# Kernel tuning notes

Hardware: AMD Instinct MI355X
Metric: run time of the kernel (lower is better)

Reference implementation:

```python
import jax, jax.numpy as jnp
import numpy as np

B, T, D, H = 4, 2048, 1024, 16
HD = D // H


def setup_inputs() -> dict:
    key = jax.random.key(0)
    ks = jax.random.split(key, 10)
    s = 1.0 / np.sqrt(D)
    # xavier_uniform bound for wbias [T,T]: sqrt(6/(T+T))
    wb_bound = float(np.sqrt(6.0 / (T + T)))
    return {
        "x": jax.random.normal(ks[0], (B, T, D), dtype=jnp.float32),
        "Wq": jax.random.normal(ks[1], (D, D), dtype=jnp.float32) * s,
        "bq": jnp.zeros((D,), dtype=jnp.float32),
        "Wk": jax.random.normal(ks[2], (D, D), dtype=jnp.float32) * s,
        "bk": jnp.zeros((D,), dtype=jnp.float32),
        "Wv": jax.random.normal(ks[3], (D, D), dtype=jnp.float32) * s,
        "bv": jnp.zeros((D,), dtype=jnp.float32),
        "Wo": jax.random.normal(ks[4], (D, D), dtype=jnp.float32) * s,
        "bo": jnp.zeros((D,), dtype=jnp.float32),
        "wbias": jax.random.uniform(ks[5], (T, T), dtype=jnp.float32,
                                    minval=-wb_bound, maxval=wb_bound),
    }


def reference(x, Wq, bq, Wk, bk, Wv, bv, Wo, bo, wbias):
    Bc, Tc, Dc = x.shape
    # projections, split heads: [B, H, T, HD]
    def proj(W, b):
        y = x @ W + b
        return y.reshape(Bc, Tc, H, HD).transpose(0, 2, 1, 3)

    Q = proj(Wq, bq)
    K = proj(Wk, bk)
    V = proj(Wv, bv)

    Q_sig = jax.nn.sigmoid(Q)
    eK = jnp.exp(K)                      # [B,H,T,HD]
    ew = jnp.exp(wbias[:Tc, :Tc])        # [T,T]

    num = jnp.einsum('ts,bhsd->bhtd', ew, eK * V)
    den = jnp.einsum('ts,bhsd->bhtd', ew, eK)
    out = Q_sig * (num / den)            # [B,H,T,HD]

    out = out.transpose(0, 2, 1, 3).reshape(Bc, Tc, Dc)
    return out @ Wo + bo
```

## Files before the change

kernel.cpp:

```cpp
#include <hip/hip_runtime.h>
#include <hip/hip_bf16.h>


#define AS1(p) ((const __attribute__((address_space(1))) void*)(p))
#define AS3(p) ((__attribute__((address_space(3))) void*)(p))

typedef _Float16 half8 __attribute__((ext_vector_type(8)));
typedef _Float16 half4v __attribute__((ext_vector_type(4)));
typedef float floatx16 __attribute__((ext_vector_type(16)));

__global__ void prep_cast_exp(const float* __restrict__ x, const float* __restrict__ wb,
                              _Float16* __restrict__ x_h, _Float16* __restrict__ ew_h) {
  int i = blockIdx.x * 256 + threadIdx.x;
  if (i < 2097152) {
    float4 v = ((const float4*)x)[i];
    half4v h;
    h[0] = (_Float16)v.x; h[1] = (_Float16)v.y; h[2] = (_Float16)v.z; h[3] = (_Float16)v.w;
    ((half4v*)x_h)[i] = h;
  } else {
    int j = i - 2097152;
    float4 v = ((const float4*)wb)[j];
    half4v h;
    h[0] = (_Float16)__expf(v.x); h[1] = (_Float16)__expf(v.y);
    h[2] = (_Float16)__expf(v.z); h[3] = (_Float16)__expf(v.w);
    ((half4v*)ew_h)[j] = h;
  }
}

__global__ void transpose_cast_w(const float* __restrict__ w0, const float* __restrict__ w1,
                                 const float* __restrict__ w2, const float* __restrict__ w3,
                                 _Float16* __restrict__ dqkv, _Float16* __restrict__ dwo) {
  const int z = blockIdx.z;
  const float* src = z == 0 ? w0 : z == 1 ? w1 : z == 2 ? w2 : w3;
  __shared__ float tile[32][33];
  const int r0 = blockIdx.x * 32, c0 = blockIdx.y * 32;
  const int tr = threadIdx.x >> 5, tc = threadIdx.x & 31;
#pragma unroll
  for (int p = 0; p < 4; ++p) {
    int rr = tr + p * 8;
    tile[rr][tc] = src[(size_t)(r0 + rr) * 1024 + c0 + tc];
  }
  __syncthreads();
#pragma unroll
  for (int p = 0; p < 4; ++p) {
    int c = c0 + tr + p * 8;
    size_t jr;
    _Float16* dst;
    if (z == 0) { jr = c; dst = dqkv; }
    else if (z == 3) { jr = c; dst = dwo; }
    else { jr = 1024 + ((size_t)(c >> 5) << 6) + ((z == 2) ? 32 : 0) + (c & 31); dst = dqkv; }
    dst[jr * 1024 + r0 + tc] = (_Float16)tile[tc][tr + p * 8];
  }
}

template <int MODE>
__global__ __launch_bounds__(256) void gemm_bt(
    const _Float16* __restrict__ A, const _Float16* __restrict__ Bt, void* __restrict__ Cv,
    int M, int N, int K, long batchB, long batchCbytes,
    const float* __restrict__ bias0, const float* __restrict__ bias1,
    const float* __restrict__ bias2, const _Float16* __restrict__ Qsig, long batchQ,
    _Float16* __restrict__ Zt) {
  __shared__ __align__(16) _Float16 sA[8192];
  __shared__ __align__(16) _Float16 sB[8192];
  const int tid = threadIdx.x;
  const int wave = tid >> 6, lane = tid & 63;
  const int l32 = lane & 31, khalf = lane >> 5;
  const int m0 = blockIdx.x * 128, n0 = blockIdx.y * 128;
  Bt += (long)blockIdx.z * batchB;
  char* Cb = (char*)Cv + (long)blockIdx.z * batchCbytes;

  const int rs = tid >> 3;
  const int ug = (tid & 7) ^ (rs & 7);
  const _Float16* gA = A + (long)(m0 + rs) * K + ug * 8;
  const _Float16* gB = Bt + (long)(n0 + rs) * K + ug * 8;
  _Float16* sAd = sA + wave * 512;
  _Float16* sBd = sB + wave * 512;

  const int wm = (wave >> 1) * 64, wn = (wave & 1) * 64;

  floatx16 acc[2][2] = {};

  for (int k0 = 0; k0 < K; k0 += 64) {
#pragma unroll
    for (int c = 0; c < 4; ++c)
      __builtin_amdgcn_global_load_lds(AS1(gA + (long)c * 32 * K + k0), AS3(sAd + c * 2048), 16,
                                       0, 0);
#pragma unroll
    for (int c = 0; c < 4; ++c)
      __builtin_amdgcn_global_load_lds(AS1(gB + (long)c * 32 * K + k0), AS3(sBd + c * 2048), 16,
                                       0, 0);
    __syncthreads();
#pragma unroll
    for (int ks = 0; ks < 4; ++ks) {
      half8 af[2], bf[2];
#pragma unroll
      for (int i = 0; i < 2; ++i) {
        int ra = wm + i * 32 + l32;
        af[i] = *(const half8*)(sA + ra * 64 + (((ks * 2 + khalf) ^ (ra & 7)) * 8));
        int rb = wn + i * 32 + l32;
        bf[i] = *(const half8*)(sB + rb * 64 + (((ks * 2 + khalf) ^ (rb & 7)) * 8));
      }
#pragma unroll
      for (int mt = 0; mt < 2; ++mt)
#pragma unroll
        for (int nt = 0; nt < 2; ++nt)
          acc[mt][nt] =
              __builtin_amdgcn_mfma_f32_32x32x16_f16(af[mt], bf[nt], acc[mt][nt], 0, 0, 0);
    }
    __syncthreads();
  }

  if (MODE == 0) {
    if (n0 < 1024) {
      _Float16* Qs = (_Float16*)Cb;
#pragma unroll
      for (int mt = 0; mt < 2; ++mt)
#pragma unroll
        for (int nt = 0; nt < 2; ++nt) {
          const int col = n0 + wn + nt * 32 + l32;
          const float bb = bias0[col];
#pragma unroll
          for (int reg = 0; reg < 16; ++reg) {
            const int row = m0 + wm + mt * 32 + 4 * khalf + 8 * (reg >> 2) + (reg & 3);
            float v = acc[mt][nt][reg] + bb;
            Qs[(long)row * 1024 + col] = (_Float16)(1.0f / (1.0f + __expf(-v)));
          }
        }
    } else {
      const int g = (n0 - 1024 + wn) >> 6;
      const int ch = g * 32 + l32;
      const float bkc = bias1[ch], bvc = bias2[ch];
#pragma unroll
      for (int mt = 0; mt < 2; ++mt) {
#pragma unroll
        for (int q = 0; q < 4; ++q) {
          half4v numv, denv;
#pragma unroll
          for (int r = 0; r < 4; ++r) {
            float ek = __expf(acc[mt][0][q * 4 + r] + bkc);
            float vv = acc[mt][1][q * 4 + r] + bvc;
            denv[r] = (_Float16)ek;
            numv[r] = (_Float16)(ek * vv);
          }
          const int row = m0 + wm + mt * 32 + 4 * khalf + 8 * q;
          const int b = row >> 11, s = row & 2047;
          const size_t jb = ((size_t)b * 2048 + (size_t)g * 64 + l32) * 2048 + s;
          *(half4v*)(Zt + jb) = numv;
          *(half4v*)(Zt + jb + 32 * 2048) = denv;
        }
      }
    }
    return;
  }

  if (MODE == 3) {
    const _Float16* Q = Qsig + (long)blockIdx.z * batchQ;
    const int ch = ((n0 + wn) >> 6) * 32 + l32;
#pragma unroll
    for (int mt = 0; mt < 2; ++mt)
#pragma unroll
      for (int reg = 0; reg < 16; ++reg) {
        const int row = m0 + wm + mt * 32 + 4 * khalf + 8 * (reg >> 2) + (reg & 3);
        float num = acc[mt][0][reg], den = acc[mt][1][reg];
        float qs = (float)Q[(long)row * 1024 + ch];
        ((_Float16*)Cb)[(long)row * 1024 + ch] = (_Float16)(qs * num / den);
      }
    return;
  }

#pragma unroll
  for (int mt = 0; mt < 2; ++mt)
#pragma unroll
    for (int nt = 0; nt < 2; ++nt) {
      const int col = n0 + wn + nt * 32 + l32;
      const float bb = bias0[col];
#pragma unroll
      for (int reg = 0; reg < 16; ++reg) {
        const int row = m0 + wm + mt * 32 + 4 * khalf + 8 * (reg >> 2) + (reg & 3);
        ((float*)Cb)[(long)row * N + col] = acc[mt][nt][reg] + bb;
      }
    }
}

extern "C" void kernel_launch(void* const* d_in, const int* in_sizes, int n_in, void* d_out,
                              int out_size, void* d_ws, size_t ws_size, hipStream_t stream) {
  const float* x = (const float*)d_in[0];
  const float* Wq = (const float*)d_in[1];
  const float* bq = (const float*)d_in[2];
  const float* Wk = (const float*)d_in[3];
  const float* bk = (const float*)d_in[4];
  const float* Wv = (const float*)d_in[5];
  const float* bv = (const float*)d_in[6];
  const float* Wo = (const float*)d_in[7];
  const float* bo = (const float*)d_in[8];
  const float* wb = (const float*)d_in[9];

  char* ws = (char*)d_ws;
  _Float16* x_h = (_Float16*)(ws + 0);
  _Float16* WqkvT = (_Float16*)(ws + 16777216);
  _Float16* WoT = (_Float16*)(ws + 23068672);
  _Float16* ew_h = (_Float16*)(ws + 25165824);
  _Float16* Qsig = (_Float16*)(ws + 33554432);
  _Float16* Zt = (_Float16*)(ws + 50331648);
  _Float16* OutHead = (_Float16*)(ws + 83886080);

  prep_cast_exp<<<12288, 256, 0, stream>>>(x, wb, x_h, ew_h);
  transpose_cast_w<<<dim3(32, 32, 4), 256, 0, stream>>>(Wq, Wk, Wv, Wo, WqkvT, WoT);

  gemm_bt<0><<<dim3(64, 24, 1), 256, 0, stream>>>(x_h, WqkvT, Qsig, 8192, 3072, 1024, 0, 0, bq,
                                                  bk, bv, nullptr, 0, Zt);

  gemm_bt<3><<<dim3(16, 16, 4), 256, 0, stream>>>(ew_h, Zt, OutHead, 2048, 2048, 2048,
                                                  (long)2048 * 2048, (long)2048 * 1024 * 2,
                                                  nullptr, nullptr, nullptr, Qsig,
                                                  (long)2048 * 1024, nullptr);

  gemm_bt<2><<<dim3(64, 8, 1), 256, 0, stream>>>(OutHead, WoT, d_out, 8192, 1024, 1024, 0, 0, bo,
                                                 nullptr, nullptr, nullptr, 0, nullptr);
}
```

Measured before the change: 302.0 us.

## Pre-tile GEMM operands into MFMA fragment order for contiguous tile loads

Every fp16 GEMM operand (x, exp(wbias), transposed weights, the num/den buffer and the per-head output) is now written in a blocked 128x64 tile layout whose element order matches the MFMA fragment order. The GEMM kernel can then fetch each K-tile with fully contiguous global-to-LDS loads and read fragments with plain lane-linear LDS reads, with no XOR swizzle or strided row addressing. The cost is scattered, narrower stores in the producer kernels and epilogues (the MODE 3 epilogue writes single halves to tiled addresses), and possible LDS bank conflicts.

Result: no change. 301.7 us (-0.1%).

```diff
diff --git a/kernel.cpp b/kernel.cpp
--- a/kernel.cpp
+++ b/kernel.cpp
@@ -9,21 +9,43 @@
 typedef _Float16 half4v __attribute__((ext_vector_type(4)));
 typedef float floatx16 __attribute__((ext_vector_type(16)));
 
-__global__ void prep_cast_exp(const float* __restrict__ x, const float* __restrict__ wb,
-                              _Float16* __restrict__ x_h, _Float16* __restrict__ ew_h) {
-  int i = blockIdx.x * 256 + threadIdx.x;
-  if (i < 2097152) {
-    float4 v = ((const float4*)x)[i];
-    half4v h;
-    h[0] = (_Float16)v.x; h[1] = (_Float16)v.y; h[2] = (_Float16)v.z; h[3] = (_Float16)v.w;
-    ((half4v*)x_h)[i] = h;
+__device__ __forceinline__ long frag_off(int r, int k) {
+  return (long)(((((r >> 5) * 4 + (k >> 4)) * 2 + ((k >> 3) & 1)) * 32 + (r & 31)) * 8 + (k & 7));
+}
+
+__global__ void prep_tiles(const float* __restrict__ x, const float* __restrict__ wb,
+                           _Float16* __restrict__ x_h, _Float16* __restrict__ ew_h) {
+  const int bid = blockIdx.x;
+  const int tid = threadIdx.x;
+  const bool isx = bid < 1024;
+  const float* src;
+  _Float16* dst;
+  int tm, tk, ld, trel;
+  if (isx) {
+    trel = bid; tm = bid >> 4; tk = bid & 15; src = x; dst = x_h; ld = 1024;
   } else {
-    int j = i - 2097152;
-    float4 v = ((const float4*)wb)[j];
-    half4v h;
-    h[0] = (_Float16)__expf(v.x); h[1] = (_Float16)__expf(v.y);
-    h[2] = (_Float16)__expf(v.z); h[3] = (_Float16)__expf(v.w);
-    ((half4v*)ew_h)[j] = h;
+    trel = bid - 1024; tm = trel >> 5; tk = trel & 31; src = wb; dst = ew_h; ld = 2048;
+  }
+  const long tbase = (long)trel * 8192;
+#pragma unroll
+  for (int p = 0; p < 4; ++p) {
+    const int s = p * 256 + tid;
+    const int r = ((s >> 8) << 5) + (s & 31);
+    const int k = ((s >> 6) & 3) * 16 + ((s >> 5) & 1) * 8;
+    const float* sp = src + (long)(tm * 128 + r) * ld + tk * 64 + k;
+    const float4 v0 = *(const float4*)sp;
+    const float4 v1 = *(const float4*)(sp + 4);
+    half8 h;
+    if (isx) {
+      h[0] = (_Float16)v0.x; h[1] = (_Float16)v0.y; h[2] = (_Float16)v0.z; h[3] = (_Float16)v0.w;
+      h[4] = (_Float16)v1.x; h[5] = (_Float16)v1.y; h[6] = (_Float16)v1.z; h[7] = (_Float16)v1.w;
+    } else {
+      h[0] = (_Float16)__expf(v0.x); h[1] = (_Float16)__expf(v0.y);
+      h[2] = (_Float16)__expf(v0.z); h[3] = (_Float16)__expf(v0.w);
+      h[4] = (_Float16)__expf(v1.x); h[5] = (_Float16)__expf(v1.y);
+      h[6] = (_Float16)__expf(v1.z); h[7] = (_Float16)__expf(v1.w);
+    }
+    *(half8*)(dst + tbase + (long)s * 8) = h;
   }
 }
 
@@ -43,22 +65,23 @@
   __syncthreads();
 #pragma unroll
   for (int p = 0; p < 4; ++p) {
-    int c = c0 + tr + p * 8;
-    size_t jr;
+    const int c = c0 + tr + p * 8;
+    const int kk = r0 + tc;
+    int jr;
     _Float16* dst;
     if (z == 0) { jr = c; dst = dqkv; }
     else if (z == 3) { jr = c; dst = dwo; }
-    else { jr = 1024 + ((size_t)(c >> 5) << 6) + ((z == 2) ? 32 : 0) + (c & 31); dst = dqkv; }
-    dst[jr * 1024 + r0 + tc] = (_Float16)tile[tc][tr + p * 8];
+    else { jr = 1024 + ((c >> 5) << 6) + ((z == 2) ? 32 : 0) + (c & 31); dst = dqkv; }
+    const long addr = ((long)(jr >> 7) * 16 + (kk >> 6)) * 8192 + frag_off(jr & 127, kk & 63);
+    dst[addr] = (_Float16)tile[tc][tr + p * 8];
   }
 }
 
 template <int MODE>
 __global__ __launch_bounds__(256) void gemm_bt(
     const _Float16* __restrict__ A, const _Float16* __restrict__ Bt, void* __restrict__ Cv,
-    int M, int N, int K, long batchB, long batchCbytes,
-    const float* __restrict__ bias0, const float* __restrict__ bias1,
-    const float* __restrict__ bias2, const _Float16* __restrict__ Qsig, long batchQ,
+    int Ktiles, long batchB, const float* __restrict__ bias0, const float* __restrict__ bias1,
+    const float* __restrict__ bias2, const _Float16* __restrict__ Qsig,
     _Float16* __restrict__ Zt) {
   __shared__ __align__(16) _Float16 sA[8192];
   __shared__ __align__(16) _Float16 sB[8192];
@@ -66,39 +89,29 @@
   const int wave = tid >> 6, lane = tid & 63;
   const int l32 = lane & 31, khalf = lane >> 5;
   const int m0 = blockIdx.x * 128, n0 = blockIdx.y * 128;
-  Bt += (long)blockIdx.z * batchB;
-  char* Cb = (char*)Cv + (long)blockIdx.z * batchCbytes;
-
-  const int rs = tid >> 3;
-  const int ug = (tid & 7) ^ (rs & 7);
-  const _Float16* gA = A + (long)(m0 + rs) * K + ug * 8;
-  const _Float16* gB = Bt + (long)(n0 + rs) * K + ug * 8;
-  _Float16* sAd = sA + wave * 512;
-  _Float16* sBd = sB + wave * 512;
-
   const int wm = (wave >> 1) * 64, wn = (wave & 1) * 64;
 
+  const _Float16* Atile = A + (long)blockIdx.x * Ktiles * 8192;
+  const _Float16* Btile = Bt + (long)blockIdx.z * batchB + (long)blockIdx.y * Ktiles * 8192;
+
   floatx16 acc[2][2] = {};
 
-  for (int k0 = 0; k0 < K; k0 += 64) {
-#pragma unroll
-    for (int c = 0; c < 4; ++c)
-      __builtin_amdgcn_global_load_lds(AS1(gA + (long)c * 32 * K + k0), AS3(sAd + c * 2048), 16,
-                                       0, 0);
-#pragma unroll
-    for (int c = 0; c < 4; ++c)
-      __builtin_amdgcn_global_load_lds(AS1(gB + (long)c * 32 * K + k0), AS3(sBd + c * 2048), 16,
-                                       0, 0);
+  for (int tk = 0; tk < Ktiles; ++tk) {
+    const _Float16* As = Atile + tk * 8192 + wave * 512 + lane * 8;
+    const _Float16* Bs = Btile + tk * 8192 + wave * 512 + lane * 8;
+#pragma unroll
+    for (int c = 0; c < 4; ++c) {
+      __builtin_amdgcn_global_load_lds(AS1(As + c * 2048), AS3(sA + c * 2048 + wave * 512), 16, 0, 0);
+      __builtin_amdgcn_global_load_lds(AS1(Bs + c * 2048), AS3(sB + c * 2048 + wave * 512), 16, 0, 0);
+    }
     __syncthreads();
 #pragma unroll
     for (int ks = 0; ks < 4; ++ks) {
       half8 af[2], bf[2];
 #pragma unroll
       for (int i = 0; i < 2; ++i) {
-        int ra = wm + i * 32 + l32;
-        af[i] = *(const half8*)(sA + ra * 64 + (((ks * 2 + khalf) ^ (ra & 7)) * 8));
-        int rb = wn + i * 32 + l32;
-        bf[i] = *(const half8*)(sB + rb * 64 + (((ks * 2 + khalf) ^ (rb & 7)) * 8));
+        af[i] = *(const half8*)(sA + (((wm >> 5) + i) * 4 + ks) * 512 + lane * 8);
+        bf[i] = *(const half8*)(sB + (((wn >> 5) + i) * 4 + ks) * 512 + lane * 8);
       }
 #pragma unroll
       for (int mt = 0; mt < 2; ++mt)
@@ -112,7 +125,7 @@
 
   if (MODE == 0) {
     if (n0 < 1024) {
-      _Float16* Qs = (_Float16*)Cb;
+      _Float16* Qs = (_Float16*)Cv;
 #pragma unroll
       for (int mt = 0; mt < 2; ++mt)
 #pragma unroll
@@ -122,7 +135,7 @@
 #pragma unroll
           for (int reg = 0; reg < 16; ++reg) {
             const int row = m0 + wm + mt * 32 + 4 * khalf + 8 * (reg >> 2) + (reg & 3);
-            float v = acc[mt][nt][reg] + bb;
+            const float v = acc[mt][nt][reg] + bb;
             Qs[(long)row * 1024 + col] = (_Float16)(1.0f / (1.0f + __expf(-v)));
           }
         }
@@ -130,23 +143,26 @@
       const int g = (n0 - 1024 + wn) >> 6;
       const int ch = g * 32 + l32;
       const float bkc = bias1[ch], bvc = bias2[ch];
+      const int jn = g * 64 + l32;
+      const long tnbase = (long)(jn >> 7) * 32 * 8192;
 #pragma unroll
       for (int mt = 0; mt < 2; ++mt) {
 #pragma unroll
         for (int q = 0; q < 4; ++q) {
           half4v numv, denv;
 #pragma unroll
-          for (int r = 0; r < 4; ++r) {
-            float ek = __expf(acc[mt][0][q * 4 + r] + bkc);
-            float vv = acc[mt][1][q * 4 + r] + bvc;
-            denv[r] = (_Float16)ek;
-            numv[r] = (_Float16)(ek * vv);
+          for (int rr = 0; rr < 4; ++rr) {
+            const float ek = __expf(acc[mt][0][q * 4 + rr] + bkc);
+            const float vv = acc[mt][1][q * 4 + rr] + bvc;
+            denv[rr] = (_Float16)ek;
+            numv[rr] = (_Float16)(ek * vv);
           }
           const int row = m0 + wm + mt * 32 + 4 * khalf + 8 * q;
           const int b = row >> 11, s = row & 2047;
-          const size_t jb = ((size_t)b * 2048 + (size_t)g * 64 + l32) * 2048 + s;
-          *(half4v*)(Zt + jb) = numv;
-          *(half4v*)(Zt + jb + 32 * 2048) = denv;
+          const long off = (long)b * 4194304 + tnbase + (long)(s >> 6) * 8192 +
+                           frag_off(jn & 127, s & 63);
+          *(half4v*)(Zt + off) = numv;
+          *(half4v*)(Zt + off + 2048) = denv;
         }
       }
     }
@@ -154,16 +170,19 @@
   }
 
   if (MODE == 3) {
-    const _Float16* Q = Qsig + (long)blockIdx.z * batchQ;
+    const _Float16* Q = Qsig + (long)blockIdx.z * 2097152;
     const int ch = ((n0 + wn) >> 6) * 32 + l32;
+    _Float16* OH = (_Float16*)Cv;
 #pragma unroll
     for (int mt = 0; mt < 2; ++mt)
 #pragma unroll
       for (int reg = 0; reg < 16; ++reg) {
-        const int row = m0 + wm + mt * 32 + 4 * khalf + 8 * (reg >> 2) + (reg & 3);
-        float num = acc[mt][0][reg], den = acc[mt][1][reg];
-        float qs = (float)Q[(long)row * 1024 + ch];
-        ((_Float16*)Cb)[(long)row * 1024 + ch] = (_Float16)(qs * num / den);
+        const int r = m0 + wm + mt * 32 + 4 * khalf + 8 * (reg >> 2) + (reg & 3);
+        const float num = acc[mt][0][reg], den = acc[mt][1][reg];
+        const float qs = (float)Q[(long)r * 1024 + ch];
+        const int R = blockIdx.z * 2048 + r;
+        const long off = ((long)(R >> 7) * 16 + (ch >> 6)) * 8192 + frag_off(R & 127, ch & 63);
+        OH[off] = (_Float16)(qs * num / den);
       }
     return;
   }
@@ -177,7 +196,7 @@
 #pragma unroll
       for (int reg = 0; reg < 16; ++reg) {
         const int row = m0 + wm + mt * 32 + 4 * khalf + 8 * (reg >> 2) + (reg & 3);
-        ((float*)Cb)[(long)row * N + col] = acc[mt][nt][reg] + bb;
+        ((float*)Cv)[(long)row * 1024 + col] = acc[mt][nt][reg] + bb;
       }
     }
 }
@@ -204,17 +223,15 @@
   _Float16* Zt = (_Float16*)(ws + 50331648);
   _Float16* OutHead = (_Float16*)(ws + 83886080);
 
-  prep_cast_exp<<<12288, 256, 0, stream>>>(x, wb, x_h, ew_h);
+  prep_tiles<<<1536, 256, 0, stream>>>(x, wb, x_h, ew_h);
   transpose_cast_w<<<dim3(32, 32, 4), 256, 0, stream>>>(Wq, Wk, Wv, Wo, WqkvT, WoT);
 
-  gemm_bt<0><<<dim3(64, 24, 1), 256, 0, stream>>>(x_h, WqkvT, Qsig, 8192, 3072, 1024, 0, 0, bq,
-                                                  bk, bv, nullptr, 0, Zt);
-
-  gemm_bt<3><<<dim3(16, 16, 4), 256, 0, stream>>>(ew_h, Zt, OutHead, 2048, 2048, 2048,
-                                                  (long)2048 * 2048, (long)2048 * 1024 * 2,
-                                                  nullptr, nullptr, nullptr, Qsig,
-                                                  (long)2048 * 1024, nullptr);
-
-  gemm_bt<2><<<dim3(64, 8, 1), 256, 0, stream>>>(OutHead, WoT, d_out, 8192, 1024, 1024, 0, 0, bo,
-                                                 nullptr, nullptr, nullptr, 0, nullptr);
-}
+  gemm_bt<0><<<dim3(64, 24, 1), 256, 0, stream>>>(x_h, WqkvT, Qsig, 16, 0, bq, bk, bv, nullptr,
+                                                  Zt);
+
+  gemm_bt<3><<<dim3(16, 16, 4), 256, 0, stream>>>(ew_h, Zt, OutHead, 32, (long)4194304, nullptr,
+                                                  nullptr, nullptr, Qsig, nullptr);
+
+  gemm_bt<2><<<dim3(64, 8, 1), 256, 0, stream>>>(OutHead, WoT, d_out, 16, 0, bo, nullptr,
+                                                 nullptr, nullptr, nullptr);
+}
```
